# Optimization experiments

Measured on AMD Instinct MI355X. Metric: run time of the kernel, lower is better.

The kernel has to match this reference:

```python
import jax, jax.numpy as jnp
import numpy as np
from jax.scipy.linalg import solve_triangular

B, T, YD, ZD, K, HID = 512, 128, 16, 32, 8, 64
JIT = 1e-5
LOG2PI = float(np.log(2.0 * np.pi))


def setup_inputs() -> dict:
    key = jax.random.key(0)
    ks = jax.random.split(key, 10)
    y = jax.random.normal(ks[0], (B, T, YD), jnp.float32)
    mask = jnp.ones((B, T), jnp.float32)
    times = jnp.arange(T, dtype=jnp.float32) * 0.1  # first timestep must be 0
    mu0 = 0.1 * jax.random.normal(ks[1], (ZD,), jnp.float32)
    Sigma0_diag = jax.random.uniform(ks[2], (ZD,), jnp.float32, 0.5, 1.0)
    H = jax.random.normal(ks[3], (YD, ZD), jnp.float32) / np.sqrt(ZD)
    R_diag = jax.random.uniform(ks[4], (YD,), jnp.float32, 0.1, 0.5)
    A_base = jax.random.normal(ks[5], (K, ZD, ZD), jnp.float32) * (0.1 / np.sqrt(ZD))
    W1 = jax.random.normal(ks[6], (ZD, HID), jnp.float32) / np.sqrt(ZD)
    b1 = jnp.zeros((HID,), jnp.float32)
    W2 = jax.random.normal(ks[7], (HID, K), jnp.float32) / np.sqrt(HID)
    b2 = jnp.zeros((K,), jnp.float32)
    Q_diag = jax.random.uniform(ks[8], (ZD,), jnp.float32, 0.05, 0.2)
    return dict(y=y, mask=mask, times=times, mu0=mu0, Sigma0_diag=Sigma0_diag,
                H=H, R_diag=R_diag, A_base=A_base, W1=W1, b1=b1, W2=W2, b2=b2,
                Q_diag=Q_diag, n_sub=2)


def reference(y, mask, times, mu0, Sigma0_diag, H, R_diag, A_base, W1, b1, W2, b2, Q_diag, n_sub):
    Bs, Ts, yd = y.shape
    zd = mu0.shape[0]
    Iz = jnp.eye(zd, dtype=y.dtype)
    Iy = jnp.eye(yd, dtype=y.dtype)
    R = jnp.diag(R_diag)
    Q = jnp.diag(Q_diag)
    dt = times[1] - times[0]
    h = dt / n_sub  # Euler substep size

    def alpha_fn(mu):  # (B,z) -> (B,K) softmax mixture weights (locally-linear)
        return jax.nn.softmax(jnp.tanh(mu @ W1 + b1) @ W2 + b2, axis=-1)

    def euler_step(mu, L):
        Sigma = L @ L.swapaxes(-1, -2)
        a = alpha_fn(mu)
        A = jnp.einsum('bk,kij->bij', a, A_base)  # (B,z,z)
        mu2 = mu + h * jnp.einsum('bij,bj->bi', A, mu)
        Sig2 = Sigma + h * (A @ Sigma + Sigma @ A.swapaxes(-1, -2) + Q)
        L2 = jnp.linalg.cholesky(Sig2 + JIT * Iz)
        return mu2, L2

    def update(mu_pred, L_pred, y_i):
        Sigma_pred = L_pred @ L_pred.swapaxes(-1, -2)
        y_pred = mu_pred @ H.T  # (B,y)
        S = jnp.einsum('ij,bjk,lk->bil', H, Sigma_pred, H) + R + JIT * Iy
        LS = jnp.linalg.cholesky(S)
        innov = y_i - y_pred
        HP = jnp.einsum('ij,bjk->bik', H, Sigma_pred)  # (B,y,z)
        Kg = jnp.linalg.solve(S, HP).swapaxes(-1, -2)  # (B,z,y) Kalman gain
        mu_u = mu_pred + jnp.einsum('bzy,by->bz', Kg, innov)
        ImKH = Iz - Kg @ H
        Sigma_u = ImKH @ Sigma_pred @ ImKH.swapaxes(-1, -2) + Kg @ R @ Kg.swapaxes(-1, -2)
        L_u = jnp.linalg.cholesky(Sigma_u + JIT * Iz)
        # MVN(loc=y_pred, scale_tril=LS).log_prob(y_i)
        w = solve_triangular(LS, innov[..., None], lower=True)[..., 0]
        lp = -0.5 * (jnp.sum(w * w, -1) + yd * LOG2PI) \
             - jnp.sum(jnp.log(jnp.diagonal(LS, axis1=-2, axis2=-1)), -1)
        return mu_u, L_u, lp

    mu_pred0 = jnp.broadcast_to(mu0, (Bs, zd))
    L_pred0 = jnp.broadcast_to(jnp.diag(jnp.sqrt(Sigma0_diag)), (Bs, zd, zd))

    def step(carry, xs):
        mu_pred, L_pred = carry
        y_i, m_i = xs
        mu_u, L_u, lp = update(mu_pred, L_pred, y_i)
        mu = m_i[:, None] * mu_u + (1.0 - m_i[:, None]) * mu_pred
        L = m_i[:, None, None] * L_u + (1.0 - m_i[:, None, None]) * L_pred
        lp = lp * m_i
        mu_n, L_n = mu, L
        for _ in range(n_sub):  # fixed substep count, structural loop
            mu_n, L_n = euler_step(mu_n, L_n)
        return (mu_n, L_n), (mu, L, lp)

    (_, _), (mus, Ls, lps) = jax.lax.scan(
        step, (mu_pred0, L_pred0), (y.swapaxes(0, 1), mask.swapaxes(0, 1)))
    log_prob = lps.sum(0)  # (B,)
    return mus, Ls, log_prob
```

## Files before the change

### kernel.cpp

```cpp
#include <hip/hip_runtime.h>
#include <math.h>

namespace {
constexpr int NB  = 512;
constexpr int NT  = 128;
constexpr int NY  = 16;
constexpr int NZ  = 32;
constexpr int NK  = 8;
constexpr int NH  = 64;
constexpr int NSUB = 2;
constexpr float FJIT = 1e-5f;
constexpr float CLOG2PI = 1.8378770664093453f;
}

__device__ __forceinline__ void chol8_1t(const float* src, int lds,
                                         float* dst, int ldd,
                                         int c0, float* sinvp) {
  float a[8][8];
  #pragma unroll
  for (int r = 0; r < 8; ++r)
    #pragma unroll
    for (int c = 0; c <= r; ++c) a[r][c] = src[(c0 + r) * lds + (c0 + c)];
  float iv[8];
  #pragma unroll
  for (int j = 0; j < 8; ++j) {
    const float d  = sqrtf(a[j][j]);
    const float id = 1.0f / d;
    iv[j] = id; a[j][j] = d;
    #pragma unroll
    for (int r = j + 1; r < 8; ++r) a[r][j] *= id;
    #pragma unroll
    for (int k = j + 1; k < 8; ++k)
      #pragma unroll
      for (int r = k; r < 8; ++r) a[r][k] -= a[r][j] * a[k][j];
  }
  #pragma unroll
  for (int r = 0; r < 8; ++r) {
    #pragma unroll
    for (int c = 0; c <= r; ++c) dst[(c0 + r) * ldd + (c0 + c)] = a[r][c];
    sinvp[c0 + r] = iv[r];
  }
}

__device__ __forceinline__ void chol8_trail_1t(const float* mat, int ld,
                                               float* dst, int ldd,
                                               int c0, float* sinvp) {
  float a[8][8];
  #pragma unroll
  for (int r = 0; r < 8; ++r)
    #pragma unroll
    for (int c = 0; c <= r; ++c) {
      float s = mat[(c0 + r) * ld + (c0 + c)];
      #pragma unroll
      for (int q = 0; q < 8; ++q)
        s -= dst[(c0 + r) * ldd + (c0 - 8 + q)] * dst[(c0 + c) * ldd + (c0 - 8 + q)];
      a[r][c] = s;
    }
  float iv[8];
  #pragma unroll
  for (int j = 0; j < 8; ++j) {
    const float d  = sqrtf(a[j][j]);
    const float id = 1.0f / d;
    iv[j] = id; a[j][j] = d;
    #pragma unroll
    for (int r = j + 1; r < 8; ++r) a[r][j] *= id;
    #pragma unroll
    for (int k = j + 1; k < 8; ++k)
      #pragma unroll
      for (int r = k; r < 8; ++r) a[r][k] -= a[r][j] * a[k][j];
  }
  #pragma unroll
  for (int r = 0; r < 8; ++r) {
    #pragma unroll
    for (int c = 0; c <= r; ++c) dst[(c0 + r) * ldd + (c0 + c)] = a[r][c];
    sinvp[c0 + r] = iv[r];
  }
}

__device__ __forceinline__ void panel_row(const float* src, int lds,
                                          float* dst, int ldd,
                                          int c0, int i, const float* sinvp) {
  float w[8];
  #pragma unroll
  for (int q = 0; q < 8; ++q) w[q] = src[i * lds + c0 + q];
  #pragma unroll
  for (int q = 0; q < 8; ++q) {
    float s = w[q];
    #pragma unroll
    for (int p = 0; p < q; ++p) s -= dst[(c0 + q) * ldd + (c0 + p)] * w[p];
    w[q] = s * sinvp[c0 + q];
  }
  #pragma unroll
  for (int q = 0; q < 8; ++q) dst[i * ldd + c0 + q] = w[q];
}

__global__ __launch_bounds__(256, 2)
void kf_scan_kernel(const float* __restrict__ gy,
                    const float* __restrict__ gmask,
                    const float* __restrict__ gtimes,
                    const float* __restrict__ gmu0,
                    const float* __restrict__ gSig0d,
                    const float* __restrict__ gH,
                    const float* __restrict__ gRd,
                    const float* __restrict__ gAb,
                    const float* __restrict__ gW1,
                    const float* __restrict__ gb1,
                    const float* __restrict__ gW2,
                    const float* __restrict__ gb2,
                    const float* __restrict__ gQd,
                    float* __restrict__ out_mus,
                    float* __restrict__ out_Ls,
                    float* __restrict__ out_lp)
{
  const int b   = blockIdx.x;
  const int tid = threadIdx.x;
  const int i8  = tid >> 3;
  const int j8  = (tid & 7) << 2;

  __shared__ float sAb[NK][NZ][NZ+1];
  __shared__ float sW1[NZ][NH];
  __shared__ float sH [NY][NZ+1];
  __shared__ float sW2[NH][NK];
  __shared__ float sb1v[NH];
  __shared__ float sb2v[NK];
  __shared__ float sRd[NY];
  __shared__ float sQd[NZ];
  __shared__ float Sig[NZ][NZ+1];
  __shared__ float Wk [NZ][NZ+1];
  __shared__ float T1 [NZ][NZ+1];
  __shared__ float T2 [NZ][NZ+1];
  __shared__ float HP [NY][NZ+1];
  __shared__ float Sm [NY][NY+1];
  __shared__ float SL [NY][NY+1];
  __shared__ float Kg [NZ][NY+1];
  __shared__ float muv[NZ], muu[NZ], innov[NY], hidv[NH], alphav[NK];
  __shared__ float siv[NZ];
  __shared__ float lpt;

  double lpacc = 0.0;

  for (int idx = tid; idx < NK*NZ*NZ; idx += 256) {
    const int k = idx >> 10, r = (idx >> 5) & 31, c = idx & 31;
    sAb[k][r][c] = gAb[idx];
  }
  for (int idx = tid; idx < NZ*NH; idx += 256) ((float*)sW1)[idx] = gW1[idx];
  for (int idx = tid; idx < NY*NZ; idx += 256) {
    const int r = idx >> 5, c = idx & 31;
    sH[r][c] = gH[idx];
  }
  for (int idx = tid; idx < NH*NK; idx += 256) ((float*)sW2)[idx] = gW2[idx];
  if (tid < NH) sb1v[tid] = gb1[tid];
  if (tid < NK) sb2v[tid] = gb2[tid];
  if (tid < NY) sRd[tid]  = gRd[tid];
  if (tid < NZ) sQd[tid]  = gQd[tid];
  if (tid < NZ) {
    muv[tid] = gmu0[tid];
    for (int j = 0; j < NZ; ++j) Sig[tid][j] = 0.0f;
    const float r = sqrtf(gSig0d[tid]);
    Sig[tid][tid] = r * r;
  }
  const float dtv = gtimes[1] - gtimes[0];
  const float h   = dtv / (float)NSUB;

  float yreg = (tid < NY) ? gy[(size_t)b*NT*NY + tid] : 0.0f;
  __syncthreads();

  #pragma unroll 1
  for (int t = 0; t < NT; ++t) {
    const float m = gmask[(size_t)b*NT + t];

    if (tid < NY) {
      float s = 0.f;
      #pragma unroll
      for (int k = 0; k < NZ; ++k) s += sH[tid][k] * muv[k];
      innov[tid] = yreg - s;
    }
    {
      const int i16 = tid >> 4, c0 = (tid & 15) << 1;
      float s0 = 0.f, s1 = 0.f;
      #pragma unroll
      for (int k = 0; k < NZ; ++k) {
        const float hv = sH[i16][k];
        s0 += hv * Sig[k][c0];
        s1 += hv * Sig[k][c0+1];
      }
      HP[i16][c0] = s0; HP[i16][c0+1] = s1;
    }
    __syncthreads();

    if (tid < NY && t + 1 < NT) yreg = gy[((size_t)b*NT + t + 1)*NY + tid];
    {
      int r, c;
      if (tid < 64)       { r = tid >> 3;              c = tid & 7; }
      else if (tid < 128) { r = (tid - 64) >> 3;       c = 8 + ((tid - 64) & 7); }
      else                { r = 8 + ((tid - 128) >> 4); c = (tid - 128) & 15; }
      float s = 0.f;
      #pragma unroll
      for (int k = 0; k < NZ; ++k) s += HP[r][k] * sH[c][k];
      if (r == c) s += sRd[r] + FJIT;
      Sm[r][c] = s;
    }
    if (tid == 0) chol8_1t(&Sm[0][0], NY+1, &SL[0][0], NY+1, 0, siv);
    __syncthreads();

    if (tid < 8) panel_row(&Sm[0][0], NY+1, &SL[0][0], NY+1, 0, 8 + tid, siv);
    __syncthreads();
    if (tid == 0) chol8_trail_1t(&Sm[0][0], NY+1, &SL[0][0], NY+1, 8, siv);
    __syncthreads();

    if (tid < NZ) {
      const int c = tid;
      float s[NY], v[NY];
      #pragma unroll
      for (int i = 0; i < NY; ++i) s[i] = HP[i][c];
      #pragma unroll
      for (int i = 0; i < NY; ++i) {
        const float vi = s[i] * siv[i];
        v[i] = vi;
        #pragma unroll
        for (int jj = i+1; jj < NY; ++jj) s[jj] -= SL[jj][i] * vi;
      }
      float x[NY];
      #pragma unroll
      for (int i = NY-1; i >= 0; --i) {
        const float xi = v[i] * siv[i];
        x[i] = xi;
        #pragma unroll
        for (int jj = 0; jj < i; ++jj) v[jj] -= SL[i][jj] * xi;
      }
      float acc = 0.f;
      #pragma unroll
      for (int i = 0; i < NY; ++i) { Kg[c][i] = x[i]; acc += x[i] * innov[i]; }
      muu[c] = muv[c] + acc;
    } else if (tid == 64) {
      float s[NY];
      #pragma unroll
      for (int i = 0; i < NY; ++i) s[i] = innov[i];
      float sw = 0.f, prod = 1.f;
      #pragma unroll
      for (int i = 0; i < NY; ++i) {
        const float wi = s[i] * siv[i];
        sw += wi * wi;
        prod *= SL[i][i];
        #pragma unroll
        for (int jj = i+1; jj < NY; ++jj) s[jj] -= SL[jj][i] * wi;
      }
      lpt = -0.5f * (sw + NY * CLOG2PI) - logf(prod);
    }
    __syncthreads();

    {
      #pragma unroll
      for (int q = 0; q < 4; ++q) {
        const int j = j8 + q;
        float s1 = (i8 == j) ? 1.0f : 0.0f;
        float s2 = Sig[i8][j];
        #pragma unroll
        for (int yy = 0; yy < NY; ++yy) {
          const float kv = Kg[i8][yy];
          s1 -= kv * sH[yy][j];
          s2 -= kv * HP[yy][j];
        }
        T1[i8][j] = s1;
        T2[i8][j] = s2;
      }
    }
    __syncthreads();

    {
      #pragma unroll
      for (int q = 0; q < 4; ++q) {
        const int j = j8 + q;
        if (j <= i8) {
          float s = 0.f;
          #pragma unroll
          for (int k = 0; k < NZ; ++k) s += T2[i8][k] * T1[j][k];
          float s2 = 0.f;
          #pragma unroll
          for (int yy = 0; yy < NY; ++yy) s2 += Kg[i8][yy] * sRd[yy] * Kg[j][yy];
          s += s2;
          if (i8 == j) s += FJIT;
          Wk[i8][j] = s;
        }
      }
    }
    if (tid == 0) chol8_1t(&Wk[0][0], NZ+1, &T2[0][0], NZ+1, 0, siv);
    __syncthreads();

    #pragma unroll 1
    for (int blkb = 0; blkb < 3; ++blkb) {
      const int c0 = blkb << 3;
      if (tid < 24 - c0) panel_row(&Wk[0][0], NZ+1, &T2[0][0], NZ+1, c0, c0 + 8 + tid, siv);
      __syncthreads();
      if (i8 >= c0 + 16) {
        #pragma unroll
        for (int q4 = 0; q4 < 4; ++q4) {
          const int k = j8 + q4;
          if (k >= c0 + 8 && k <= i8) {
            float s = Wk[i8][k];
            #pragma unroll
            for (int q = 0; q < 8; ++q) s -= T2[i8][c0+q] * T2[k][c0+q];
            Wk[i8][k] = s;
          }
        }
      }
      if (tid == 0) chol8_trail_1t(&Wk[0][0], NZ+1, &T2[0][0], NZ+1, c0 + 8, siv);
      __syncthreads();
    }

    if (tid < NZ) {
      const float nm = m * muu[tid] + (1.0f - m) * muv[tid];
      out_mus[((size_t)t*NB + b)*NZ + tid] = nm;
      muv[tid] = nm;
    }
    if (tid == 0) lpacc += (double)(m * lpt);
    {
      float4 lv;
      lv.x = (j8+0 <= i8) ? T2[i8][j8+0] : 0.0f;
      lv.y = (j8+1 <= i8) ? T2[i8][j8+1] : 0.0f;
      lv.z = (j8+2 <= i8) ? T2[i8][j8+2] : 0.0f;
      lv.w = (j8+3 <= i8) ? T2[i8][j8+3] : 0.0f;
      *(float4*)&out_Ls[(((size_t)t*NB + b)*NZ + i8)*NZ + j8] = lv;
      #pragma unroll
      for (int q = 0; q < 4; ++q) {
        const int j = j8 + q;
        const int km = (i8 < j) ? i8 : j;
        float s = 0.f;
        for (int k = 0; k <= km; ++k) s += T2[i8][k] * T2[j][k];
        Sig[i8][j] = s;
      }
    }
    if (tid < NH) {
      __builtin_amdgcn_sched_barrier(0);
      float sacc = sb1v[tid];
      #pragma unroll
      for (int k = 0; k < NZ; ++k) sacc += muv[k] * sW1[k][tid];
      hidv[tid] = tanhf(sacc);
      __builtin_amdgcn_sched_barrier(0);
      const int kk = tid & 7, r0 = (tid >> 3) << 3;
      float part = 0.f;
      #pragma unroll
      for (int j = 0; j < 8; ++j) part += hidv[r0 + j] * sW2[r0 + j][kk];
      part += __shfl_xor(part, 8);
      part += __shfl_xor(part, 16);
      part += __shfl_xor(part, 32);
      float lg[NK];
      #pragma unroll
      for (int q = 0; q < NK; ++q) lg[q] = __shfl(part, (tid & 56) | q) + sb2v[q];
      float mx = lg[0];
      #pragma unroll
      for (int q = 1; q < NK; ++q) mx = fmaxf(mx, lg[q]);
      float se = 0.f;
      #pragma unroll
      for (int q = 0; q < NK; ++q) { lg[q] = expf(lg[q] - mx); se += lg[q]; }
      const float inv = 1.0f / se;
      if (tid == 0) {
        #pragma unroll
        for (int q = 0; q < NK; ++q) alphav[q] = lg[q] * inv;
      }
    }
    __syncthreads();

    #pragma unroll 1
    for (int ss = 0; ss < NSUB; ++ss) {
      {
        #pragma unroll
        for (int q = 0; q < 4; ++q) {
          const int j = j8 + q;
          float s = 0.f;
          #pragma unroll
          for (int k = 0; k < NK; ++k) s += alphav[k] * sAb[k][i8][j];
          T1[i8][j] = s;
        }
      }
      __syncthreads();
      if (tid < NZ) {
        float s = 0.f;
        #pragma unroll
        for (int k = 0; k < NZ; ++k) s += T1[tid][k] * muv[k];
        muu[tid] = muv[tid] + h * s;
      }
      {
        float a0=0.f, a1=0.f, a2=0.f, a3=0.f;
        #pragma unroll
        for (int k = 0; k < NZ; ++k) {
          const float a = T1[i8][k];
          a0 += a * Sig[k][j8];
          a1 += a * Sig[k][j8+1];
          a2 += a * Sig[k][j8+2];
          a3 += a * Sig[k][j8+3];
        }
        T2[i8][j8] = a0; T2[i8][j8+1] = a1; T2[i8][j8+2] = a2; T2[i8][j8+3] = a3;
      }
      __syncthreads();
      {
        #pragma unroll
        for (int q = 0; q < 4; ++q) {
          const int j = j8 + q;
          float s = Sig[i8][j] + h * (T2[i8][j] + T2[j][i8]);
          if (i8 == j) s += h * sQd[i8] + FJIT;
          Sig[i8][j] = s;
        }
      }
      if (tid < NZ) muv[tid] = muu[tid];
      if (ss == 0 && tid < NH) {
        __builtin_amdgcn_sched_barrier(0);
        float sacc = sb1v[tid];
        #pragma unroll
        for (int k = 0; k < NZ; ++k) sacc += muv[k] * sW1[k][tid];
        hidv[tid] = tanhf(sacc);
        __builtin_amdgcn_sched_barrier(0);
        const int kk = tid & 7, r0 = (tid >> 3) << 3;
        float part = 0.f;
        #pragma unroll
        for (int j = 0; j < 8; ++j) part += hidv[r0 + j] * sW2[r0 + j][kk];
        part += __shfl_xor(part, 8);
        part += __shfl_xor(part, 16);
        part += __shfl_xor(part, 32);
        float lg[NK];
        #pragma unroll
        for (int q = 0; q < NK; ++q) lg[q] = __shfl(part, (tid & 56) | q) + sb2v[q];
        float mx = lg[0];
        #pragma unroll
        for (int q = 1; q < NK; ++q) mx = fmaxf(mx, lg[q]);
        float se = 0.f;
        #pragma unroll
        for (int q = 0; q < NK; ++q) { lg[q] = expf(lg[q] - mx); se += lg[q]; }
        const float inv = 1.0f / se;
        if (tid == 0) {
          #pragma unroll
          for (int q = 0; q < NK; ++q) alphav[q] = lg[q] * inv;
        }
      }
      __syncthreads();
    }
  }

  if (tid == 0) out_lp[b] = (float)lpacc;
}

extern "C" void kernel_launch(void* const* d_in, const int* in_sizes, int n_in,
                              void* d_out, int out_size, void* d_ws, size_t ws_size,
                              hipStream_t stream) {
  (void)in_sizes; (void)n_in; (void)d_ws; (void)ws_size; (void)out_size;
  const float* gy     = (const float*)d_in[0];
  const float* gmask  = (const float*)d_in[1];
  const float* gtimes = (const float*)d_in[2];
  const float* gmu0   = (const float*)d_in[3];
  const float* gS0d   = (const float*)d_in[4];
  const float* gH     = (const float*)d_in[5];
  const float* gRd    = (const float*)d_in[6];
  const float* gAb    = (const float*)d_in[7];
  const float* gW1    = (const float*)d_in[8];
  const float* gb1    = (const float*)d_in[9];
  const float* gW2    = (const float*)d_in[10];
  const float* gb2    = (const float*)d_in[11];
  const float* gQd    = (const float*)d_in[12];

  float* out = (float*)d_out;
  float* out_mus = out;
  float* out_Ls  = out + (size_t)NT*NB*NZ;
  float* out_lp  = out + (size_t)NT*NB*NZ + (size_t)NT*NB*NZ*NZ;

  kf_scan_kernel<<<NB, 256, 0, stream>>>(gy, gmask, gtimes, gmu0, gS0d, gH, gRd,
                                         gAb, gW1, gb1, gW2, gb2, gQd,
                                         out_mus, out_Ls, out_lp);
}
```

Baseline: 3.794 ms.

## Drop shared A_base, vectorize LDS with padded strides, raise occupancy

Removes the 33KB shared copy of A_base and reads the mixture matrices directly from global memory as float4 in each Euler substep, shrinking LDS use so launch bounds can request 4 blocks per CU. All shared matrices use 36/20-float row strides with 16-byte alignment, so inner products and updates become float4 LDS loads and stores. The Cholesky output's upper triangle is zeroed explicitly, which lets the L·Lᵀ reconstruction and the L store run without branches. Risks include global-load latency on A_base every substep, more bank conflicts from the new strides, and register pressure under the tighter launch bound.

```diff
diff --git a/kernel.cpp b/kernel.cpp
--- a/kernel.cpp
+++ b/kernel.cpp
@@ -9,6 +9,8 @@
 constexpr int NK  = 8;
 constexpr int NH  = 64;
 constexpr int NSUB = 2;
+constexpr int SZ  = 36;
+constexpr int SY  = 20;
 constexpr float FJIT = 1e-5f;
 constexpr float CLOG2PI = 1.8378770664093453f;
 }
@@ -94,7 +96,7 @@
   for (int q = 0; q < 8; ++q) dst[i * ldd + c0 + q] = w[q];
 }
 
-__global__ __launch_bounds__(256, 2)
+__global__ __launch_bounds__(256, 4)
 void kf_scan_kernel(const float* __restrict__ gy,
                     const float* __restrict__ gmask,
                     const float* __restrict__ gtimes,
@@ -117,32 +119,28 @@
   const int i8  = tid >> 3;
   const int j8  = (tid & 7) << 2;
 
-  __shared__ float sAb[NK][NZ][NZ+1];
-  __shared__ float sW1[NZ][NH];
-  __shared__ float sH [NY][NZ+1];
+  __shared__ alignas(16) float sW1[NZ][NH];
+  __shared__ alignas(16) float sH [NY][SZ];
   __shared__ float sW2[NH][NK];
   __shared__ float sb1v[NH];
   __shared__ float sb2v[NK];
-  __shared__ float sRd[NY];
+  __shared__ alignas(16) float sRd[NY];
   __shared__ float sQd[NZ];
-  __shared__ float Sig[NZ][NZ+1];
-  __shared__ float Wk [NZ][NZ+1];
-  __shared__ float T1 [NZ][NZ+1];
-  __shared__ float T2 [NZ][NZ+1];
-  __shared__ float HP [NY][NZ+1];
-  __shared__ float Sm [NY][NY+1];
-  __shared__ float SL [NY][NY+1];
-  __shared__ float Kg [NZ][NY+1];
-  __shared__ float muv[NZ], muu[NZ], innov[NY], hidv[NH], alphav[NK];
+  __shared__ alignas(16) float Sig[NZ][SZ];
+  __shared__ alignas(16) float Wk [NZ][SZ];
+  __shared__ alignas(16) float T1 [NZ][SZ];
+  __shared__ alignas(16) float T2 [NZ][SZ];
+  __shared__ alignas(16) float HP [NY][SZ];
+  __shared__ float Sm[NY][NY+1];
+  __shared__ float SL[NY][NY+1];
+  __shared__ alignas(16) float Kg[NZ][SY];
+  __shared__ alignas(16) float muv[NZ];
+  __shared__ float muu[NZ], innov[NY], hidv[NH], alphav[NK];
   __shared__ float siv[NZ];
   __shared__ float lpt;
 
   double lpacc = 0.0;
 
-  for (int idx = tid; idx < NK*NZ*NZ; idx += 256) {
-    const int k = idx >> 10, r = (idx >> 5) & 31, c = idx & 31;
-    sAb[k][r][c] = gAb[idx];
-  }
   for (int idx = tid; idx < NZ*NH; idx += 256) ((float*)sW1)[idx] = gW1[idx];
   for (int idx = tid; idx < NY*NZ; idx += 256) {
     const int r = idx >> 5, c = idx & 31;
@@ -172,7 +170,11 @@
     if (tid < NY) {
       float s = 0.f;
       #pragma unroll
-      for (int k = 0; k < NZ; ++k) s += sH[tid][k] * muv[k];
+      for (int kb = 0; kb < 8; ++kb) {
+        const float4 h4 = *(const float4*)&sH[tid][kb*4];
+        const float4 m4 = *(const float4*)&muv[kb*4];
+        s += h4.x*m4.x; s += h4.y*m4.y; s += h4.z*m4.z; s += h4.w*m4.w;
+      }
       innov[tid] = yreg - s;
     }
     {
@@ -181,8 +183,9 @@
       #pragma unroll
       for (int k = 0; k < NZ; ++k) {
         const float hv = sH[i16][k];
-        s0 += hv * Sig[k][c0];
-        s1 += hv * Sig[k][c0+1];
+        const float2 sg = *(const float2*)&Sig[k][c0];
+        s0 += hv * sg.x;
+        s1 += hv * sg.y;
       }
       HP[i16][c0] = s0; HP[i16][c0+1] = s1;
     }
@@ -196,7 +199,11 @@
       else                { r = 8 + ((tid - 128) >> 4); c = (tid - 128) & 15; }
       float s = 0.f;
       #pragma unroll
-      for (int k = 0; k < NZ; ++k) s += HP[r][k] * sH[c][k];
+      for (int kb = 0; kb < 8; ++kb) {
+        const float4 a4 = *(const float4*)&HP[r][kb*4];
+        const float4 b4 = *(const float4*)&sH[c][kb*4];
+        s += a4.x*b4.x; s += a4.y*b4.y; s += a4.z*b4.z; s += a4.w*b4.w;
+      }
       if (r == c) s += sRd[r] + FJIT;
       Sm[r][c] = s;
     }
@@ -230,7 +237,10 @@
       }
       float acc = 0.f;
       #pragma unroll
-      for (int i = 0; i < NY; ++i) { Kg[c][i] = x[i]; acc += x[i] * innov[i]; }
+      for (int i = 0; i < NY; ++i) acc += x[i] * innov[i];
+      #pragma unroll
+      for (int yb = 0; yb < 4; ++yb)
+        *(float4*)&Kg[c][yb*4] = make_float4(x[yb*4], x[yb*4+1], x[yb*4+2], x[yb*4+3]);
       muu[c] = muv[c] + acc;
     } else if (tid == 64) {
       float s[NY];
@@ -250,47 +260,81 @@
     __syncthreads();
 
     {
+      float kr[16];
+      #pragma unroll
+      for (int yb = 0; yb < 4; ++yb) {
+        const float4 v = *(const float4*)&Kg[i8][yb*4];
+        kr[yb*4] = v.x; kr[yb*4+1] = v.y; kr[yb*4+2] = v.z; kr[yb*4+3] = v.w;
+      }
+      float4 s1v = make_float4((i8==j8)?1.f:0.f, (i8==j8+1)?1.f:0.f,
+                               (i8==j8+2)?1.f:0.f, (i8==j8+3)?1.f:0.f);
+      float4 s2v = *(const float4*)&Sig[i8][j8];
+      #pragma unroll
+      for (int yy = 0; yy < NY; ++yy) {
+        const float kv = kr[yy];
+        const float4 h4 = *(const float4*)&sH[yy][j8];
+        const float4 p4 = *(const float4*)&HP[yy][j8];
+        s1v.x -= kv*h4.x; s1v.y -= kv*h4.y; s1v.z -= kv*h4.z; s1v.w -= kv*h4.w;
+        s2v.x -= kv*p4.x; s2v.y -= kv*p4.y; s2v.z -= kv*p4.z; s2v.w -= kv*p4.w;
+      }
+      *(float4*)&T1[i8][j8] = s1v;
+      *(float4*)&T2[i8][j8] = s2v;
+    }
+    __syncthreads();
+
+    {
+      float t2r[NZ];
+      #pragma unroll
+      for (int kb = 0; kb < 8; ++kb) {
+        const float4 v = *(const float4*)&T2[i8][kb*4];
+        t2r[kb*4] = v.x; t2r[kb*4+1] = v.y; t2r[kb*4+2] = v.z; t2r[kb*4+3] = v.w;
+      }
+      float kr[16];
+      #pragma unroll
+      for (int yb = 0; yb < 4; ++yb) {
+        const float4 v = *(const float4*)&Kg[i8][yb*4];
+        kr[yb*4] = v.x; kr[yb*4+1] = v.y; kr[yb*4+2] = v.z; kr[yb*4+3] = v.w;
+      }
+      float rdr[16];
+      #pragma unroll
+      for (int yb = 0; yb < 4; ++yb) {
+        const float4 v = *(const float4*)&sRd[yb*4];
+        rdr[yb*4] = v.x; rdr[yb*4+1] = v.y; rdr[yb*4+2] = v.z; rdr[yb*4+3] = v.w;
+      }
+      float4 wv;
+      float* wvp = &wv.x;
       #pragma unroll
       for (int q = 0; q < 4; ++q) {
         const int j = j8 + q;
-        float s1 = (i8 == j) ? 1.0f : 0.0f;
-        float s2 = Sig[i8][j];
-        #pragma unroll
-        for (int yy = 0; yy < NY; ++yy) {
-          const float kv = Kg[i8][yy];
-          s1 -= kv * sH[yy][j];
-          s2 -= kv * HP[yy][j];
-        }
-        T1[i8][j] = s1;
-        T2[i8][j] = s2;
-      }
-    }
-    __syncthreads();
-
-    {
-      #pragma unroll
-      for (int q = 0; q < 4; ++q) {
-        const int j = j8 + q;
-        if (j <= i8) {
-          float s = 0.f;
-          #pragma unroll
-          for (int k = 0; k < NZ; ++k) s += T2[i8][k] * T1[j][k];
-          float s2 = 0.f;
-          #pragma unroll
-          for (int yy = 0; yy < NY; ++yy) s2 += Kg[i8][yy] * sRd[yy] * Kg[j][yy];
-          s += s2;
-          if (i8 == j) s += FJIT;
-          Wk[i8][j] = s;
-        }
-      }
-    }
-    if (tid == 0) chol8_1t(&Wk[0][0], NZ+1, &T2[0][0], NZ+1, 0, siv);
+        float s = 0.f;
+        #pragma unroll
+        for (int kb = 0; kb < 8; ++kb) {
+          const float4 t1v = *(const float4*)&T1[j][kb*4];
+          s += t2r[kb*4]*t1v.x; s += t2r[kb*4+1]*t1v.y;
+          s += t2r[kb*4+2]*t1v.z; s += t2r[kb*4+3]*t1v.w;
+        }
+        float s2 = 0.f;
+        #pragma unroll
+        for (int yb = 0; yb < 4; ++yb) {
+          const float4 kg4 = *(const float4*)&Kg[j][yb*4];
+          s2 += kr[yb*4]*rdr[yb*4]*kg4.x;
+          s2 += kr[yb*4+1]*rdr[yb*4+1]*kg4.y;
+          s2 += kr[yb*4+2]*rdr[yb*4+2]*kg4.z;
+          s2 += kr[yb*4+3]*rdr[yb*4+3]*kg4.w;
+        }
+        s += s2;
+        if (i8 == j) s += FJIT;
+        wvp[q] = s;
+      }
+      *(float4*)&Wk[i8][j8] = wv;
+    }
+    if (tid == 0) chol8_1t(&Wk[0][0], SZ, &T2[0][0], SZ, 0, siv);
     __syncthreads();
 
     #pragma unroll 1
     for (int blkb = 0; blkb < 3; ++blkb) {
       const int c0 = blkb << 3;
-      if (tid < 24 - c0) panel_row(&Wk[0][0], NZ+1, &T2[0][0], NZ+1, c0, c0 + 8 + tid, siv);
+      if (tid < 24 - c0) panel_row(&Wk[0][0], SZ, &T2[0][0], SZ, c0, c0 + 8 + tid, siv);
       __syncthreads();
       if (i8 >= c0 + 16) {
         #pragma unroll
@@ -304,7 +348,12 @@
           }
         }
       }
-      if (tid == 0) chol8_trail_1t(&Wk[0][0], NZ+1, &T2[0][0], NZ+1, c0 + 8, siv);
+      if (blkb == 2) {
+        #pragma unroll
+        for (int q = 0; q < 4; ++q)
+          if (j8 + q > i8) T2[i8][j8+q] = 0.f;
+      }
+      if (tid == 0) chol8_trail_1t(&Wk[0][0], SZ, &T2[0][0], SZ, c0 + 8, siv);
       __syncthreads();
     }
 
@@ -315,20 +364,29 @@
     }
     if (tid == 0) lpacc += (double)(m * lpt);
     {
-      float4 lv;
-      lv.x = (j8+0 <= i8) ? T2[i8][j8+0] : 0.0f;
-      lv.y = (j8+1 <= i8) ? T2[i8][j8+1] : 0.0f;
-      lv.z = (j8+2 <= i8) ? T2[i8][j8+2] : 0.0f;
-      lv.w = (j8+3 <= i8) ? T2[i8][j8+3] : 0.0f;
+      const float4 lv = *(const float4*)&T2[i8][j8];
       *(float4*)&out_Ls[(((size_t)t*NB + b)*NZ + i8)*NZ + j8] = lv;
+      float t2r[NZ];
+      #pragma unroll
+      for (int kb = 0; kb < 8; ++kb) {
+        const float4 v = *(const float4*)&T2[i8][kb*4];
+        t2r[kb*4] = v.x; t2r[kb*4+1] = v.y; t2r[kb*4+2] = v.z; t2r[kb*4+3] = v.w;
+      }
+      float4 sv;
+      float* svp = &sv.x;
       #pragma unroll
       for (int q = 0; q < 4; ++q) {
         const int j = j8 + q;
-        const int km = (i8 < j) ? i8 : j;
         float s = 0.f;
-        for (int k = 0; k <= km; ++k) s += T2[i8][k] * T2[j][k];
-        Sig[i8][j] = s;
-      }
+        #pragma unroll
+        for (int kb = 0; kb < 8; ++kb) {
+          const float4 l4 = *(const float4*)&T2[j][kb*4];
+          s += t2r[kb*4]*l4.x; s += t2r[kb*4+1]*l4.y;
+          s += t2r[kb*4+2]*l4.z; s += t2r[kb*4+3]*l4.w;
+        }
+        svp[q] = s;
+      }
+      *(float4*)&Sig[i8][j8] = sv;
     }
     if (tid < NH) {
       __builtin_amdgcn_sched_barrier(0);
@@ -364,43 +422,56 @@
     #pragma unroll 1
     for (int ss = 0; ss < NSUB; ++ss) {
       {
-        #pragma unroll
-        for (int q = 0; q < 4; ++q) {
-          const int j = j8 + q;
-          float s = 0.f;
-          #pragma unroll
-          for (int k = 0; k < NK; ++k) s += alphav[k] * sAb[k][i8][j];
-          T1[i8][j] = s;
-        }
+        const float* gp = gAb + (size_t)i8*NZ + j8;
+        float4 ab[NK];
+        #pragma unroll
+        for (int k = 0; k < NK; ++k) ab[k] = *(const float4*)(gp + (size_t)k*NZ*NZ);
+        float4 a4 = make_float4(0.f, 0.f, 0.f, 0.f);
+        #pragma unroll
+        for (int k = 0; k < NK; ++k) {
+          const float al = alphav[k];
+          a4.x += al*ab[k].x; a4.y += al*ab[k].y;
+          a4.z += al*ab[k].z; a4.w += al*ab[k].w;
+        }
+        *(float4*)&T1[i8][j8] = a4;
       }
       __syncthreads();
       if (tid < NZ) {
         float s = 0.f;
         #pragma unroll
-        for (int k = 0; k < NZ; ++k) s += T1[tid][k] * muv[k];
+        for (int kb = 0; kb < 8; ++kb) {
+          const float4 t14 = *(const float4*)&T1[tid][kb*4];
+          const float4 m4  = *(const float4*)&muv[kb*4];
+          s += t14.x*m4.x; s += t14.y*m4.y; s += t14.z*m4.z; s += t14.w*m4.w;
+        }
         muu[tid] = muv[tid] + h * s;
       }
       {
-        float a0=0.f, a1=0.f, a2=0.f, a3=0.f;
+        float4 acc = make_float4(0.f, 0.f, 0.f, 0.f);
         #pragma unroll
         for (int k = 0; k < NZ; ++k) {
           const float a = T1[i8][k];
-          a0 += a * Sig[k][j8];
-          a1 += a * Sig[k][j8+1];
-          a2 += a * Sig[k][j8+2];
-          a3 += a * Sig[k][j8+3];
-        }
-        T2[i8][j8] = a0; T2[i8][j8+1] = a1; T2[i8][j8+2] = a2; T2[i8][j8+3] = a3;
+          const float4 sg = *(const float4*)&Sig[k][j8];
+          acc.x += a*sg.x; acc.y += a*sg.y; acc.z += a*sg.z; acc.w += a*sg.w;
+        }
+        *(float4*)&T2[i8][j8] = acc;
       }
       __syncthreads();
       {
-        #pragma unroll
-        for (int q = 0; q < 4; ++q) {
-          const int j = j8 + q;
-          float s = Sig[i8][j] + h * (T2[i8][j] + T2[j][i8]);
-          if (i8 == j) s += h * sQd[i8] + FJIT;
-          Sig[i8][j] = s;
-        }
+        const float4 tv = *(const float4*)&T2[i8][j8];
+        float tT[4];
+        #pragma unroll
+        for (int q = 0; q < 4; ++q) tT[q] = T2[j8+q][i8];
+        float4 sg = *(const float4*)&Sig[i8][j8];
+        sg.x += h * (tv.x + tT[0]);
+        sg.y += h * (tv.y + tT[1]);
+        sg.z += h * (tv.z + tT[2]);
+        sg.w += h * (tv.w + tT[3]);
+        float* sgp = &sg.x;
+        #pragma unroll
+        for (int q = 0; q < 4; ++q)
+          if (i8 == j8 + q) sgp[q] += h * sQd[i8] + FJIT;
+        *(float4*)&Sig[i8][j8] = sg;
       }
       if (tid < NZ) muv[tid] = muu[tid];
       if (ss == 0 && tid < NH) {
```

Result: slower. 5.092 ms (+34.2%).

## Overlap mean/MLP/A-matrix chain with Cholesky panel steps on idle wavefront

Applied to the files above, without the earlier changes.

Moves the mean update, both MLP softmax-weight evaluations, the two mean Euler substeps and the construction of both mixed A matrices onto the last wavefront (threads 192-255). This work now runs during the serial Cholesky panel and trailing phases of the update step, where most threads were idle. The substep loop then only does the covariance propagation using the precomputed A matrices (T1 and a new TB buffer), which removes several barriers per timestep. The substep count is hardcoded to 2, and the added shared buffer and register arrays raise resource use.

```diff
diff --git a/kernel.cpp b/kernel.cpp
--- a/kernel.cpp
+++ b/kernel.cpp
@@ -8,7 +8,6 @@
 constexpr int NZ  = 32;
 constexpr int NK  = 8;
 constexpr int NH  = 64;
-constexpr int NSUB = 2;
 constexpr float FJIT = 1e-5f;
 constexpr float CLOG2PI = 1.8378770664093453f;
 }
@@ -92,6 +91,36 @@
   }
   #pragma unroll
   for (int q = 0; q < 8; ++q) dst[i * ldd + c0 + q] = w[q];
+}
+
+__device__ __forceinline__ void w3_mlp_alphas(int l, const float* mu_in,
+                                              float* hid, const float* W1,
+                                              const float* b1, const float* W2,
+                                              const float* b2, float* al) {
+  float sacc = b1[l];
+  #pragma unroll
+  for (int k = 0; k < NZ; ++k) sacc += mu_in[k] * W1[k * NH + l];
+  hid[l] = tanhf(sacc);
+  __builtin_amdgcn_sched_barrier(0);
+  const int kk = l & 7, r0 = (l >> 3) << 3;
+  float part = 0.f;
+  #pragma unroll
+  for (int j = 0; j < 8; ++j) part += hid[r0 + j] * W2[(r0 + j) * NK + kk];
+  part += __shfl_xor(part, 8);
+  part += __shfl_xor(part, 16);
+  part += __shfl_xor(part, 32);
+  float lg[NK];
+  #pragma unroll
+  for (int q = 0; q < NK; ++q) lg[q] = __shfl(part, (l & 56) | q) + b2[q];
+  float mx = lg[0];
+  #pragma unroll
+  for (int q = 1; q < NK; ++q) mx = fmaxf(mx, lg[q]);
+  float se = 0.f;
+  #pragma unroll
+  for (int q = 0; q < NK; ++q) { lg[q] = expf(lg[q] - mx); se += lg[q]; }
+  const float inv = 1.0f / se;
+  #pragma unroll
+  for (int q = 0; q < NK; ++q) al[q] = lg[q] * inv;
 }
 
 __global__ __launch_bounds__(256, 2)
@@ -129,11 +158,12 @@
   __shared__ float Wk [NZ][NZ+1];
   __shared__ float T1 [NZ][NZ+1];
   __shared__ float T2 [NZ][NZ+1];
+  __shared__ float TB [NZ][NZ+1];
   __shared__ float HP [NY][NZ+1];
-  __shared__ float Sm [NY][NY+1];
-  __shared__ float SL [NY][NY+1];
-  __shared__ float Kg [NZ][NY+1];
-  __shared__ float muv[NZ], muu[NZ], innov[NY], hidv[NH], alphav[NK];
+  __shared__ float Sm[NY][NY+1];
+  __shared__ float SL[NY][NY+1];
+  __shared__ float Kg[NZ][NY+1];
+  __shared__ float muv[NZ], muu[NZ], innov[NY], hidv[NH];
   __shared__ float siv[NZ];
   __shared__ float lpt;
 
@@ -160,7 +190,7 @@
     Sig[tid][tid] = r * r;
   }
   const float dtv = gtimes[1] - gtimes[0];
-  const float h   = dtv / (float)NSUB;
+  const float h   = dtv / 2.0f;
 
   float yreg = (tid < NY) ? gy[(size_t)b*NT*NY + tid] : 0.0f;
   __syncthreads();
@@ -287,32 +317,77 @@
     if (tid == 0) chol8_1t(&Wk[0][0], NZ+1, &T2[0][0], NZ+1, 0, siv);
     __syncthreads();
 
-    #pragma unroll 1
+    float al0[NK], al1[NK];
+    #pragma unroll
     for (int blkb = 0; blkb < 3; ++blkb) {
       const int c0 = blkb << 3;
-      if (tid < 24 - c0) panel_row(&Wk[0][0], NZ+1, &T2[0][0], NZ+1, c0, c0 + 8 + tid, siv);
+      if (tid < 24 - c0) {
+        panel_row(&Wk[0][0], NZ+1, &T2[0][0], NZ+1, c0, c0 + 8 + tid, siv);
+      } else if (tid >= 192) {
+        const int l = tid - 192;
+        if (blkb == 0) {
+          if (l < NZ) {
+            const float nm = m * muu[l] + (1.0f - m) * muv[l];
+            out_mus[((size_t)t*NB + b)*NZ + l] = nm;
+            muv[l] = nm;
+          }
+          __builtin_amdgcn_sched_barrier(0);
+          w3_mlp_alphas(l, muv, hidv, &sW1[0][0], sb1v, &sW2[0][0], sb2v, al0);
+        } else if (blkb == 1) {
+          if (l < NZ) {
+            float s = 0.f;
+            #pragma unroll
+            for (int k = 0; k < NZ; ++k) s += T1[l][k] * muv[k];
+            muu[l] = muv[l] + h * s;
+          }
+          __builtin_amdgcn_sched_barrier(0);
+          w3_mlp_alphas(l, muu, hidv, &sW1[0][0], sb1v, &sW2[0][0], sb2v, al1);
+        } else {
+          if (l < NZ) {
+            float s = 0.f;
+            #pragma unroll
+            for (int k = 0; k < NZ; ++k) s += TB[l][k] * muu[k];
+            muv[l] = muu[l] + h * s;
+          }
+        }
+      }
       __syncthreads();
-      if (i8 >= c0 + 16) {
-        #pragma unroll
-        for (int q4 = 0; q4 < 4; ++q4) {
-          const int k = j8 + q4;
-          if (k >= c0 + 8 && k <= i8) {
-            float s = Wk[i8][k];
-            #pragma unroll
-            for (int q = 0; q < 8; ++q) s -= T2[i8][c0+q] * T2[k][c0+q];
-            Wk[i8][k] = s;
+      {
+        const int nr = (16 - c0) << 3;
+        if (tid >= 8 && tid < 8 + nr) {
+          const int rr = c0 + 16 + ((tid - 8) >> 3);
+          const int jq = ((tid - 8) & 7) << 2;
+          #pragma unroll
+          for (int q4 = 0; q4 < 4; ++q4) {
+            const int k = jq + q4;
+            if (k >= c0 + 8 && k <= rr) {
+              float s = Wk[rr][k];
+              #pragma unroll
+              for (int q = 0; q < 8; ++q) s -= T2[rr][c0+q] * T2[k][c0+q];
+              Wk[rr][k] = s;
+            }
           }
         }
       }
-      if (tid == 0) chol8_trail_1t(&Wk[0][0], NZ+1, &T2[0][0], NZ+1, c0 + 8, siv);
+      if (tid == 0) {
+        chol8_trail_1t(&Wk[0][0], NZ+1, &T2[0][0], NZ+1, c0 + 8, siv);
+      } else if (tid >= 192 && blkb < 2) {
+        const int l = tid - 192;
+        const float* al = (blkb == 0) ? al0 : al1;
+        float* Adst = (blkb == 0) ? &T1[0][0] : &TB[0][0];
+        #pragma unroll
+        for (int e = 0; e < 16; ++e) {
+          const int idx = (l << 4) + e;
+          const int r = idx >> 5, c = idx & 31;
+          float s = 0.f;
+          #pragma unroll
+          for (int k = 0; k < NK; ++k) s += al[k] * sAb[k][r][c];
+          Adst[r * (NZ+1) + c] = s;
+        }
+      }
       __syncthreads();
     }
 
-    if (tid < NZ) {
-      const float nm = m * muu[tid] + (1.0f - m) * muv[tid];
-      out_mus[((size_t)t*NB + b)*NZ + tid] = nm;
-      muv[tid] = nm;
-    }
     if (tid == 0) lpacc += (double)(m * lpt);
     {
       float4 lv;
@@ -330,61 +405,16 @@
         Sig[i8][j] = s;
       }
     }
-    if (tid < NH) {
-      __builtin_amdgcn_sched_barrier(0);
-      float sacc = sb1v[tid];
-      #pragma unroll
-      for (int k = 0; k < NZ; ++k) sacc += muv[k] * sW1[k][tid];
-      hidv[tid] = tanhf(sacc);
-      __builtin_amdgcn_sched_barrier(0);
-      const int kk = tid & 7, r0 = (tid >> 3) << 3;
-      float part = 0.f;
-      #pragma unroll
-      for (int j = 0; j < 8; ++j) part += hidv[r0 + j] * sW2[r0 + j][kk];
-      part += __shfl_xor(part, 8);
-      part += __shfl_xor(part, 16);
-      part += __shfl_xor(part, 32);
-      float lg[NK];
-      #pragma unroll
-      for (int q = 0; q < NK; ++q) lg[q] = __shfl(part, (tid & 56) | q) + sb2v[q];
-      float mx = lg[0];
-      #pragma unroll
-      for (int q = 1; q < NK; ++q) mx = fmaxf(mx, lg[q]);
-      float se = 0.f;
-      #pragma unroll
-      for (int q = 0; q < NK; ++q) { lg[q] = expf(lg[q] - mx); se += lg[q]; }
-      const float inv = 1.0f / se;
-      if (tid == 0) {
-        #pragma unroll
-        for (int q = 0; q < NK; ++q) alphav[q] = lg[q] * inv;
-      }
-    }
-    __syncthreads();
-
-    #pragma unroll 1
-    for (int ss = 0; ss < NSUB; ++ss) {
-      {
-        #pragma unroll
-        for (int q = 0; q < 4; ++q) {
-          const int j = j8 + q;
-          float s = 0.f;
-          #pragma unroll
-          for (int k = 0; k < NK; ++k) s += alphav[k] * sAb[k][i8][j];
-          T1[i8][j] = s;
-        }
-      }
-      __syncthreads();
-      if (tid < NZ) {
-        float s = 0.f;
-        #pragma unroll
-        for (int k = 0; k < NZ; ++k) s += T1[tid][k] * muv[k];
-        muu[tid] = muv[tid] + h * s;
-      }
+    __syncthreads();
+
+    #pragma unroll
+    for (int ss = 0; ss < 2; ++ss) {
+      const float (*A)[NZ+1] = (ss == 0) ? T1 : TB;
       {
         float a0=0.f, a1=0.f, a2=0.f, a3=0.f;
         #pragma unroll
         for (int k = 0; k < NZ; ++k) {
-          const float a = T1[i8][k];
+          const float a = A[i8][k];
           a0 += a * Sig[k][j8];
           a1 += a * Sig[k][j8+1];
           a2 += a * Sig[k][j8+2];
@@ -400,36 +430,6 @@
           float s = Sig[i8][j] + h * (T2[i8][j] + T2[j][i8]);
           if (i8 == j) s += h * sQd[i8] + FJIT;
           Sig[i8][j] = s;
-        }
-      }
-      if (tid < NZ) muv[tid] = muu[tid];
-      if (ss == 0 && tid < NH) {
-        __builtin_amdgcn_sched_barrier(0);
-        float sacc = sb1v[tid];
-        #pragma unroll
-        for (int k = 0; k < NZ; ++k) sacc += muv[k] * sW1[k][tid];
-        hidv[tid] = tanhf(sacc);
-        __builtin_amdgcn_sched_barrier(0);
-        const int kk = tid & 7, r0 = (tid >> 3) << 3;
-        float part = 0.f;
-        #pragma unroll
-        for (int j = 0; j < 8; ++j) part += hidv[r0 + j] * sW2[r0 + j][kk];
-        part += __shfl_xor(part, 8);
-        part += __shfl_xor(part, 16);
-        part += __shfl_xor(part, 32);
-        float lg[NK];
-        #pragma unroll
-        for (int q = 0; q < NK; ++q) lg[q] = __shfl(part, (tid & 56) | q) + sb2v[q];
-        float mx = lg[0];
-        #pragma unroll
-        for (int q = 1; q < NK; ++q) mx = fmaxf(mx, lg[q]);
-        float se = 0.f;
-        #pragma unroll
-        for (int q = 0; q < NK; ++q) { lg[q] = expf(lg[q] - mx); se += lg[q]; }
-        const float inv = 1.0f / se;
-        if (tid == 0) {
-          #pragma unroll
-          for (int q = 0; q < NK; ++q) alphav[q] = lg[q] * inv;
         }
       }
       __syncthreads();
```

After: 4.785 ms. 1.26x slower.
